# Kernel optimization log

Hardware: AMD Instinct MI355X
Metric: run time of the kernel (lower is better)

## Reference

```python
import jax, jax.numpy as jnp
import numpy as np

N_EMB = 384
BLOCK = 128

def setup_inputs() -> dict:
    key = jax.random.key(0)
    k1, k2, k3, k4 = jax.random.split(key, 4)
    B, T, hs = 1024, 128, 64
    x = jax.random.normal(k1, (B, T, N_EMB), dtype=jnp.float32)
    Wk = jax.random.normal(k2, (hs, N_EMB), dtype=jnp.float32) * (N_EMB ** -0.5)
    Wq = jax.random.normal(k3, (hs, N_EMB), dtype=jnp.float32) * (N_EMB ** -0.5)
    Wv = jax.random.normal(k4, (hs, N_EMB), dtype=jnp.float32) * (N_EMB ** -0.5)
    return {"x": x, "Wk": Wk, "Wq": Wq, "Wv": Wv}

def reference(x, Wk, Wq, Wv):
    B, T, C = x.shape
    # nn.Linear(n_emb, head_size, bias=False): y = x @ W.T
    k = jnp.einsum('btc,hc->bth', x, Wk)  # [B,T,hs]
    q = jnp.einsum('btc,hc->bth', x, Wq)
    v = jnp.einsum('btc,hc->bth', x, Wv)
    # NOTE: source scales by C**-0.5 where C = n_emb (384), not head_size
    w = jnp.einsum('bth,bsh->bts', q, k) * (C ** -0.5)  # [B,T,T]
    causal = jnp.tril(jnp.ones((T, T), dtype=bool))
    w = jnp.where(causal, w, -jnp.inf)
    w = jax.nn.softmax(w, axis=-1)
    # dropout is identity in eval mode
    out = jnp.einsum('bts,bsh->bth', w, v)  # [B,T,hs]
    return out
```

## Files before the change

kernel.cpp:

```cpp
#include <hip/hip_runtime.h>

typedef __bf16 bf16_t;
typedef __attribute__((ext_vector_type(8))) __bf16 bf16x8;
typedef __attribute__((ext_vector_type(4))) float floatx4;

#define MFMA16(a, b, c) __builtin_amdgcn_mfma_f32_16x16x32_bf16((a), (b), (c), 0, 0, 0)
#define GLOAD_LDS(g, l)                                                                      \
    __builtin_amdgcn_global_load_lds((const __attribute__((address_space(1))) unsigned int*)(g), \
                                     (__attribute__((address_space(3))) unsigned int*)(l), 16, 0, 0)

constexpr int TT = 128;
constexpr int CD = 384;
constexpr int HS = 64;
constexpr int BB = 1024;
constexpr int NCH = 12;

constexpr int XB0 = 0, XB1 = 17408, WB0 = 34816, WB1 = 47104;
constexpr int SMEM_BYTES = 59392;

constexpr int QK_STR = 72;
constexpr int VT_STR = 136;
constexpr int QS_OFF = 0;
constexpr int KS_OFF = TT * QK_STR;
constexpr int VT_OFF = 2 * TT * QK_STR;
constexpr int PS_OFF = 0;

__global__ void wconv_kernel(const float* __restrict__ wq, const float* __restrict__ wk,
                             const float* __restrict__ wv, bf16_t* __restrict__ wf) {
    const int t = blockIdx.x * 256 + threadIdx.x;
    if (t >= 144 * 64) return;
    const int lane = t & 63;
    const int f    = t >> 6;
    const int nt   = f & 3;
    const int proj = (f >> 2) % 3;
    const int kki  = f / 12;
    const float* W = (proj == 0) ? wq : ((proj == 1) ? wk : wv);
    const int h = 16 * nt + (lane & 15);
    const int c = 32 * kki + 8 * (lane >> 4);
    const float* src = W + h * CD + c;
    bf16x8 o;
#pragma unroll
    for (int j = 0; j < 8; ++j) o[j] = (bf16_t)src[j];
    *(bf16x8*)(wf + (size_t)t * 8) = o;
}

__launch_bounds__(256, 2)
__global__ void attn_kernel(const float* __restrict__ x, const bf16_t* __restrict__ wf,
                            float* __restrict__ out) {
    __shared__ __align__(16) char smem_raw[SMEM_BYTES];
    bf16_t* smem = (bf16_t*)smem_raw;
    const int b    = blockIdx.x;
    const int lane = threadIdx.x & 63;
    const int w    = threadIdx.x >> 6;
    const int l15  = lane & 15;
    const int g    = lane >> 4;
    const char* xb  = (const char*)(x + (size_t)b * TT * CD);
    const char* wfb = (const char*)wf;

    int      xi[5];
    unsigned xg[5];
#pragma unroll
    for (int t2 = 0; t2 < 5; ++t2) {
        const int i = w + 4 * t2;
        xi[t2] = i;
        unsigned u   = (unsigned)i * 1024u + (unsigned)lane * 16u;
        unsigned p   = u / 272u;
        unsigned rem = u - 272u * p;
        unsigned row = 2u * p + (rem >> 7);
        xg[t2] = (rem < 256u) ? row * (CD * 4u) + (rem & 127u) : 0u;
    }

    auto stage = [&](int c) {
        const char* xsrc = xb + c * 128;
        char*       xd   = smem_raw + ((c & 1) ? XB1 : XB0);
#pragma unroll
        for (int t2 = 0; t2 < 5; ++t2)
            if (xi[t2] <= 16) GLOAD_LDS(xsrc + xg[t2], xd + xi[t2] * 1024);
        const char* wsrc = wfb + (size_t)(c * 12 + 3 * w) * 1024 + (size_t)lane * 16;
        char*       wd   = smem_raw + ((c & 1) ? WB1 : WB0) + 3 * w * 1024;
#pragma unroll
        for (int j = 0; j < 3; ++j) GLOAD_LDS(wsrc + (size_t)j * 1024, wd + j * 1024);
    };

    floatx4 accq[2][4], acck[2][4], accv[2][4];
#pragma unroll
    for (int mt = 0; mt < 2; ++mt)
#pragma unroll
        for (int nt = 0; nt < 4; ++nt) {
            accq[mt][nt] = (floatx4)0.0f;
            acck[mt][nt] = (floatx4)0.0f;
            accv[mt][nt] = (floatx4)0.0f;
        }

    stage(0);
    __syncthreads();

    for (int c = 0; c < NCH; ++c) {
        if (c + 1 < NCH) stage(c + 1);

        const char*   xs = smem_raw + ((c & 1) ? XB1 : XB0);
        const char*   ws = smem_raw + ((c & 1) ? WB1 : WB0);

        bf16x8 a[2];
#pragma unroll
        for (int mt = 0; mt < 2; ++mt) {
            const int   R = 32 * w + 16 * mt + l15;
            const char* p = xs + (R >> 1) * 272 + (R & 1) * 128 + 32 * g;
            float4 f0 = *(const float4*)p;
            float4 f1 = *(const float4*)(p + 16);
            bf16x8 t;
            t[0] = (bf16_t)f0.x; t[1] = (bf16_t)f0.y; t[2] = (bf16_t)f0.z; t[3] = (bf16_t)f0.w;
            t[4] = (bf16_t)f1.x; t[5] = (bf16_t)f1.y; t[6] = (bf16_t)f1.z; t[7] = (bf16_t)f1.w;
            a[mt] = t;
        }
        bf16x8 wbf[12];
#pragma unroll
        for (int pn = 0; pn < 12; ++pn)
            wbf[pn] = *(const bf16x8*)(ws + pn * 1024 + lane * 16);
#pragma unroll
        for (int nt = 0; nt < 4; ++nt) {
            accq[0][nt] = MFMA16(a[0], wbf[0 + nt], accq[0][nt]);
            accq[1][nt] = MFMA16(a[1], wbf[0 + nt], accq[1][nt]);
            acck[0][nt] = MFMA16(a[0], wbf[4 + nt], acck[0][nt]);
            acck[1][nt] = MFMA16(a[1], wbf[4 + nt], acck[1][nt]);
            accv[0][nt] = MFMA16(a[0], wbf[8 + nt], accv[0][nt]);
            accv[1][nt] = MFMA16(a[1], wbf[8 + nt], accv[1][nt]);
        }
        __syncthreads();
    }

#pragma unroll
    for (int mt = 0; mt < 2; ++mt)
#pragma unroll
        for (int nt = 0; nt < 4; ++nt) {
            const int t0 = 32 * w + 16 * mt + 4 * g;
            const int h  = 16 * nt + l15;
#pragma unroll
            for (int r = 0; r < 4; ++r) {
                smem[QS_OFF + (t0 + r) * QK_STR + h] = (bf16_t)accq[mt][nt][r];
                smem[KS_OFF + (t0 + r) * QK_STR + h] = (bf16_t)acck[mt][nt][r];
                smem[VT_OFF + h * VT_STR + t0 + r]   = (bf16_t)accv[mt][nt][r];
            }
        }
    __syncthreads();

    floatx4 sacc[2][8];
#pragma unroll
    for (int mt = 0; mt < 2; ++mt)
#pragma unroll
        for (int nt = 0; nt < 8; ++nt) sacc[mt][nt] = (floatx4)0.0f;

#pragma unroll
    for (int kt = 0; kt < 2; ++kt) {
        const int hh = 32 * kt + 8 * g;
        bf16x8 aq[2];
        aq[0] = *(const bf16x8*)(smem + QS_OFF + (32 * w + l15) * QK_STR + hh);
        aq[1] = *(const bf16x8*)(smem + QS_OFF + (32 * w + 16 + l15) * QK_STR + hh);
#pragma unroll
        for (int nt = 0; nt < 8; ++nt) {
            if (16 * nt <= 32 * w + 31) {
                bf16x8 bk = *(const bf16x8*)(smem + KS_OFF + (16 * nt + l15) * QK_STR + hh);
                if (16 * nt <= 32 * w + 15) sacc[0][nt] = MFMA16(aq[0], bk, sacc[0][nt]);
                sacc[1][nt] = MFMA16(aq[1], bk, sacc[1][nt]);
            }
        }
    }
    __syncthreads();

    const float scale = 0.05103103630798287f;
#pragma unroll
    for (int mt = 0; mt < 2; ++mt) {
#pragma unroll
        for (int r = 0; r < 4; ++r) {
            const int t = 32 * w + 16 * mt + 4 * g + r;
            float vals[8];
            float vmax = -__builtin_inff();
#pragma unroll
            for (int nt = 0; nt < 8; ++nt) {
                const int s = 16 * nt + l15;
                float v = (s <= t) ? sacc[mt][nt][r] * scale : -__builtin_inff();
                vals[nt] = v;
                vmax = fmaxf(vmax, v);
            }
            vmax = fmaxf(vmax, __shfl_xor(vmax, 1));
            vmax = fmaxf(vmax, __shfl_xor(vmax, 2));
            vmax = fmaxf(vmax, __shfl_xor(vmax, 4));
            vmax = fmaxf(vmax, __shfl_xor(vmax, 8));
            float sum = 0.0f;
#pragma unroll
            for (int nt = 0; nt < 8; ++nt) {
                float e = __expf(vals[nt] - vmax);
                vals[nt] = e;
                sum += e;
            }
            sum += __shfl_xor(sum, 1);
            sum += __shfl_xor(sum, 2);
            sum += __shfl_xor(sum, 4);
            sum += __shfl_xor(sum, 8);
            const float inv = 1.0f / sum;
#pragma unroll
            for (int nt = 0; nt < 8; ++nt)
                smem[PS_OFF + t * VT_STR + 16 * nt + l15] = (bf16_t)(vals[nt] * inv);
        }
    }

    floatx4 oacc[2][4];
#pragma unroll
    for (int mt = 0; mt < 2; ++mt)
#pragma unroll
        for (int nt = 0; nt < 4; ++nt) oacc[mt][nt] = (floatx4)0.0f;

    for (int st = 0; st <= w; ++st) {
        const int ss = 32 * st + 8 * g;
        bf16x8 ap0 = *(const bf16x8*)(smem + PS_OFF + (32 * w + l15) * VT_STR + ss);
        bf16x8 ap1 = *(const bf16x8*)(smem + PS_OFF + (32 * w + 16 + l15) * VT_STR + ss);
#pragma unroll
        for (int nt = 0; nt < 4; ++nt) {
            bf16x8 bv = *(const bf16x8*)(smem + VT_OFF + (16 * nt + l15) * VT_STR + ss);
            oacc[0][nt] = MFMA16(ap0, bv, oacc[0][nt]);
            oacc[1][nt] = MFMA16(ap1, bv, oacc[1][nt]);
        }
    }

    float* ob = out + (size_t)b * TT * HS;
#pragma unroll
    for (int mt = 0; mt < 2; ++mt)
#pragma unroll
        for (int nt = 0; nt < 4; ++nt) {
            const int t0 = 32 * w + 16 * mt + 4 * g;
            const int h  = 16 * nt + l15;
#pragma unroll
            for (int r = 0; r < 4; ++r)
                ob[(size_t)(t0 + r) * HS + h] = oacc[mt][nt][r];
        }
}

extern "C" void kernel_launch(void* const* d_in, const int* in_sizes, int n_in,
                              void* d_out, int out_size, void* d_ws, size_t ws_size,
                              hipStream_t stream) {
    const float* x  = (const float*)d_in[0];
    const float* wk = (const float*)d_in[1];
    const float* wq = (const float*)d_in[2];
    const float* wv = (const float*)d_in[3];
    float* out = (float*)d_out;

    bf16_t* wf = (bf16_t*)d_ws;

    wconv_kernel<<<36, 256, 0, stream>>>(wq, wk, wv, wf);
    attn_kernel<<<BB, 256, 0, stream>>>(x, wf, out);
}
```

Baseline: 306.5 us.

## Make attention kernel persistent over two batches and prefetch the next batch's x

The grid is halved so each workgroup processes two batch elements in sequence. While the first batch is in its projection tail, the first x chunk of the second batch is prefetched into an extra LDS region, so the next projection can start without a cold load. The staging pipeline now uses explicit vmcnt waits and raw barriers, and prefetches two chunks ahead. LDS per block grows to about 75 KB, which may lower occupancy. The hand-tuned wait counts are fragile if the number of issued loads changes.

```diff
diff --git a/kernel.cpp b/kernel.cpp
--- a/kernel.cpp
+++ b/kernel.cpp
@@ -8,15 +8,20 @@
 #define GLOAD_LDS(g, l)                                                                      \
     __builtin_amdgcn_global_load_lds((const __attribute__((address_space(1))) unsigned int*)(g), \
                                      (__attribute__((address_space(3))) unsigned int*)(l), 16, 0, 0)
+#define WAITV(N) asm volatile("s_waitcnt vmcnt(" #N ")" ::: "memory")
+#define WAITL0() asm volatile("s_waitcnt lgkmcnt(0)" ::: "memory")
+#define BAR() __builtin_amdgcn_s_barrier()
+#define PIN() __builtin_amdgcn_sched_barrier(0)
 
 constexpr int TT = 128;
 constexpr int CD = 384;
 constexpr int HS = 64;
 constexpr int BB = 1024;
 constexpr int NCH = 12;
-
-constexpr int XB0 = 0, XB1 = 17408, WB0 = 34816, WB1 = 47104;
-constexpr int SMEM_BYTES = 59392;
+constexpr int GRID = 512;
+
+constexpr int XB0 = 0, XB1 = 17408, WB0 = 34816, WB1 = 47104, XPF = 59392;
+constexpr int SMEM_BYTES = 76800;
 
 constexpr int QK_STR = 72;
 constexpr int VT_STR = 136;
@@ -49,12 +54,10 @@
                             float* __restrict__ out) {
     __shared__ __align__(16) char smem_raw[SMEM_BYTES];
     bf16_t* smem = (bf16_t*)smem_raw;
-    const int b    = blockIdx.x;
     const int lane = threadIdx.x & 63;
     const int w    = threadIdx.x >> 6;
     const int l15  = lane & 15;
     const int g    = lane >> 4;
-    const char* xb  = (const char*)(x + (size_t)b * TT * CD);
     const char* wfb = (const char*)wf;
 
     int      xi[5];
@@ -70,169 +73,212 @@
         xg[t2] = (rem < 256u) ? row * (CD * 4u) + (rem & 127u) : 0u;
     }
 
-    auto stage = [&](int c) {
-        const char* xsrc = xb + c * 128;
-        char*       xd   = smem_raw + ((c & 1) ? XB1 : XB0);
+    auto stage_x = [&](const char* xsrc, int boff) {
+        char* xd = smem_raw + boff;
 #pragma unroll
         for (int t2 = 0; t2 < 5; ++t2)
             if (xi[t2] <= 16) GLOAD_LDS(xsrc + xg[t2], xd + xi[t2] * 1024);
+    };
+    auto stage_w = [&](int c, int boff) {
         const char* wsrc = wfb + (size_t)(c * 12 + 3 * w) * 1024 + (size_t)lane * 16;
-        char*       wd   = smem_raw + ((c & 1) ? WB1 : WB0) + 3 * w * 1024;
+        char*       wd   = smem_raw + boff + 3 * w * 1024;
 #pragma unroll
         for (int j = 0; j < 3; ++j) GLOAD_LDS(wsrc + (size_t)j * 1024, wd + j * 1024);
     };
 
-    floatx4 accq[2][4], acck[2][4], accv[2][4];
-#pragma unroll
-    for (int mt = 0; mt < 2; ++mt)
-#pragma unroll
-        for (int nt = 0; nt < 4; ++nt) {
-            accq[mt][nt] = (floatx4)0.0f;
-            acck[mt][nt] = (floatx4)0.0f;
-            accv[mt][nt] = (floatx4)0.0f;
-        }
-
-    stage(0);
-    __syncthreads();
-
-    for (int c = 0; c < NCH; ++c) {
-        if (c + 1 < NCH) stage(c + 1);
-
-        const char*   xs = smem_raw + ((c & 1) ? XB1 : XB0);
-        const char*   ws = smem_raw + ((c & 1) ? WB1 : WB0);
-
-        bf16x8 a[2];
+    const char* xb0 = (const char*)(x + (size_t)blockIdx.x * TT * CD);
+    const char* xb1 = (const char*)(x + (size_t)(blockIdx.x + GRID) * TT * CD);
+
+    stage_x(xb0, XB0);
+    stage_w(0, WB0);
+    PIN();
+    stage_x(xb0 + 128, XB1);
+    stage_w(1, WB1);
+
+#pragma unroll 1
+    for (int it = 0; it < 2; ++it) {
+        const int   b    = blockIdx.x + it * GRID;
+        const char* xcur = it ? xb1 : xb0;
+
+        floatx4 accq[2][4], acck[2][4], accv[2][4];
+#pragma unroll
+        for (int mt = 0; mt < 2; ++mt)
+#pragma unroll
+            for (int nt = 0; nt < 4; ++nt) {
+                accq[mt][nt] = (floatx4)0.0f;
+                acck[mt][nt] = (floatx4)0.0f;
+                accv[mt][nt] = (floatx4)0.0f;
+            }
+
+        if (w == 0) WAITV(8); else WAITV(7);
+        BAR();
+
+#pragma unroll 1
+        for (int c = 0; c < NCH; ++c) {
+            const char* xs = (it == 1 && c == 0) ? smem_raw + XPF
+                                                 : smem_raw + ((c & 1) ? XB1 : XB0);
+            const char* ws = smem_raw + ((c & 1) ? WB1 : WB0);
+
+            bf16x8 a[2];
+#pragma unroll
+            for (int mt = 0; mt < 2; ++mt) {
+                const int   R = 32 * w + 16 * mt + l15;
+                const char* p = xs + (R >> 1) * 272 + (R & 1) * 128 + 32 * g;
+                float4 f0 = *(const float4*)p;
+                float4 f1 = *(const float4*)(p + 16);
+                bf16x8 t;
+                t[0] = (bf16_t)f0.x; t[1] = (bf16_t)f0.y; t[2] = (bf16_t)f0.z; t[3] = (bf16_t)f0.w;
+                t[4] = (bf16_t)f1.x; t[5] = (bf16_t)f1.y; t[6] = (bf16_t)f1.z; t[7] = (bf16_t)f1.w;
+                a[mt] = t;
+            }
+            bf16x8 wbf[12];
+#pragma unroll
+            for (int pn = 0; pn < 12; ++pn)
+                wbf[pn] = *(const bf16x8*)(ws + pn * 1024 + lane * 16);
+#pragma unroll
+            for (int nt = 0; nt < 4; ++nt) {
+                accq[0][nt] = MFMA16(a[0], wbf[0 + nt], accq[0][nt]);
+                accq[1][nt] = MFMA16(a[1], wbf[0 + nt], accq[1][nt]);
+                acck[0][nt] = MFMA16(a[0], wbf[4 + nt], acck[0][nt]);
+                acck[1][nt] = MFMA16(a[1], wbf[4 + nt], acck[1][nt]);
+                accv[0][nt] = MFMA16(a[0], wbf[8 + nt], accv[0][nt]);
+                accv[1][nt] = MFMA16(a[1], wbf[8 + nt], accv[1][nt]);
+            }
+
+            WAITL0();
+            BAR();
+            if (c <= 9) {
+                stage_x(xcur + (c + 2) * 128, (c & 1) ? XB1 : XB0);
+                stage_w(c + 2, (c & 1) ? WB1 : WB0);
+                if (w == 0) WAITV(8); else WAITV(7);
+                BAR();
+            } else if (c == 10) {
+                if (it == 0) {
+                    stage_x(xb1, XPF);
+                    if (w == 0) WAITV(5); else WAITV(4);
+                } else {
+                    WAITV(0);
+                }
+                BAR();
+            }
+        }
+
+#pragma unroll
+        for (int mt = 0; mt < 2; ++mt)
+#pragma unroll
+            for (int nt = 0; nt < 4; ++nt) {
+                const int t0 = 32 * w + 16 * mt + 4 * g;
+                const int h  = 16 * nt + l15;
+#pragma unroll
+                for (int r = 0; r < 4; ++r) {
+                    smem[QS_OFF + (t0 + r) * QK_STR + h] = (bf16_t)accq[mt][nt][r];
+                    smem[KS_OFF + (t0 + r) * QK_STR + h] = (bf16_t)acck[mt][nt][r];
+                    smem[VT_OFF + h * VT_STR + t0 + r]   = (bf16_t)accv[mt][nt][r];
+                }
+            }
+        WAITL0();
+        BAR();
+
+        floatx4 sacc[2][8];
+#pragma unroll
+        for (int mt = 0; mt < 2; ++mt)
+#pragma unroll
+            for (int nt = 0; nt < 8; ++nt) sacc[mt][nt] = (floatx4)0.0f;
+
+#pragma unroll
+        for (int kt = 0; kt < 2; ++kt) {
+            const int hh = 32 * kt + 8 * g;
+            bf16x8 aq[2];
+            aq[0] = *(const bf16x8*)(smem + QS_OFF + (32 * w + l15) * QK_STR + hh);
+            aq[1] = *(const bf16x8*)(smem + QS_OFF + (32 * w + 16 + l15) * QK_STR + hh);
+#pragma unroll
+            for (int nt = 0; nt < 8; ++nt) {
+                if (16 * nt <= 32 * w + 31) {
+                    bf16x8 bk = *(const bf16x8*)(smem + KS_OFF + (16 * nt + l15) * QK_STR + hh);
+                    if (16 * nt <= 32 * w + 15) sacc[0][nt] = MFMA16(aq[0], bk, sacc[0][nt]);
+                    sacc[1][nt] = MFMA16(aq[1], bk, sacc[1][nt]);
+                }
+            }
+        }
+        WAITL0();
+        BAR();
+
+        const float scale = 0.05103103630798287f;
 #pragma unroll
         for (int mt = 0; mt < 2; ++mt) {
-            const int   R = 32 * w + 16 * mt + l15;
-            const char* p = xs + (R >> 1) * 272 + (R & 1) * 128 + 32 * g;
-            float4 f0 = *(const float4*)p;
-            float4 f1 = *(const float4*)(p + 16);
-            bf16x8 t;
-            t[0] = (bf16_t)f0.x; t[1] = (bf16_t)f0.y; t[2] = (bf16_t)f0.z; t[3] = (bf16_t)f0.w;
-            t[4] = (bf16_t)f1.x; t[5] = (bf16_t)f1.y; t[6] = (bf16_t)f1.z; t[7] = (bf16_t)f1.w;
-            a[mt] = t;
-        }
-        bf16x8 wbf[12];
-#pragma unroll
-        for (int pn = 0; pn < 12; ++pn)
-            wbf[pn] = *(const bf16x8*)(ws + pn * 1024 + lane * 16);
-#pragma unroll
-        for (int nt = 0; nt < 4; ++nt) {
-            accq[0][nt] = MFMA16(a[0], wbf[0 + nt], accq[0][nt]);
-            accq[1][nt] = MFMA16(a[1], wbf[0 + nt], accq[1][nt]);
-            acck[0][nt] = MFMA16(a[0], wbf[4 + nt], acck[0][nt]);
-            acck[1][nt] = MFMA16(a[1], wbf[4 + nt], acck[1][nt]);
-            accv[0][nt] = MFMA16(a[0], wbf[8 + nt], accv[0][nt]);
-            accv[1][nt] = MFMA16(a[1], wbf[8 + nt], accv[1][nt]);
-        }
-        __syncthreads();
+#pragma unroll
+            for (int r = 0; r < 4; ++r) {
+                const int t = 32 * w + 16 * mt + 4 * g + r;
+                float vals[8];
+                float vmax = -__builtin_inff();
+#pragma unroll
+                for (int nt = 0; nt < 8; ++nt) {
+                    const int s = 16 * nt + l15;
+                    float v = (s <= t) ? sacc[mt][nt][r] * scale : -__builtin_inff();
+                    vals[nt] = v;
+                    vmax = fmaxf(vmax, v);
+                }
+                vmax = fmaxf(vmax, __shfl_xor(vmax, 1));
+                vmax = fmaxf(vmax, __shfl_xor(vmax, 2));
+                vmax = fmaxf(vmax, __shfl_xor(vmax, 4));
+                vmax = fmaxf(vmax, __shfl_xor(vmax, 8));
+                float sum = 0.0f;
+#pragma unroll
+                for (int nt = 0; nt < 8; ++nt) {
+                    float e = __expf(vals[nt] - vmax);
+                    vals[nt] = e;
+                    sum += e;
+                }
+                sum += __shfl_xor(sum, 1);
+                sum += __shfl_xor(sum, 2);
+                sum += __shfl_xor(sum, 4);
+                sum += __shfl_xor(sum, 8);
+                const float inv = 1.0f / sum;
+#pragma unroll
+                for (int nt = 0; nt < 8; ++nt)
+                    smem[PS_OFF + t * VT_STR + 16 * nt + l15] = (bf16_t)(vals[nt] * inv);
+            }
+        }
+
+        floatx4 oacc[2][4];
+#pragma unroll
+        for (int mt = 0; mt < 2; ++mt)
+#pragma unroll
+            for (int nt = 0; nt < 4; ++nt) oacc[mt][nt] = (floatx4)0.0f;
+
+        for (int st = 0; st <= w; ++st) {
+            const int ss = 32 * st + 8 * g;
+            bf16x8 ap0 = *(const bf16x8*)(smem + PS_OFF + (32 * w + l15) * VT_STR + ss);
+            bf16x8 ap1 = *(const bf16x8*)(smem + PS_OFF + (32 * w + 16 + l15) * VT_STR + ss);
+#pragma unroll
+            for (int nt = 0; nt < 4; ++nt) {
+                bf16x8 bv = *(const bf16x8*)(smem + VT_OFF + (16 * nt + l15) * VT_STR + ss);
+                oacc[0][nt] = MFMA16(ap0, bv, oacc[0][nt]);
+                oacc[1][nt] = MFMA16(ap1, bv, oacc[1][nt]);
+            }
+        }
+
+        float* ob = out + (size_t)b * TT * HS;
+#pragma unroll
+        for (int mt = 0; mt < 2; ++mt)
+#pragma unroll
+            for (int nt = 0; nt < 4; ++nt) {
+                const int t0 = 32 * w + 16 * mt + 4 * g;
+                const int h  = 16 * nt + l15;
+#pragma unroll
+                for (int r = 0; r < 4; ++r)
+                    ob[(size_t)(t0 + r) * HS + h] = oacc[mt][nt][r];
+            }
+
+        if (it == 0) {
+            WAITL0();
+            BAR();
+            stage_w(0, WB0);
+            PIN();
+            stage_x(xb1 + 128, XB1);
+            stage_w(1, WB1);
+        }
     }
-
-#pragma unroll
-    for (int mt = 0; mt < 2; ++mt)
-#pragma unroll
-        for (int nt = 0; nt < 4; ++nt) {
-            const int t0 = 32 * w + 16 * mt + 4 * g;
-            const int h  = 16 * nt + l15;
-#pragma unroll
-            for (int r = 0; r < 4; ++r) {
-                smem[QS_OFF + (t0 + r) * QK_STR + h] = (bf16_t)accq[mt][nt][r];
-                smem[KS_OFF + (t0 + r) * QK_STR + h] = (bf16_t)acck[mt][nt][r];
-                smem[VT_OFF + h * VT_STR + t0 + r]   = (bf16_t)accv[mt][nt][r];
-            }
-        }
-    __syncthreads();
-
-    floatx4 sacc[2][8];
-#pragma unroll
-    for (int mt = 0; mt < 2; ++mt)
-#pragma unroll
-        for (int nt = 0; nt < 8; ++nt) sacc[mt][nt] = (floatx4)0.0f;
-
-#pragma unroll
-    for (int kt = 0; kt < 2; ++kt) {
-        const int hh = 32 * kt + 8 * g;
-        bf16x8 aq[2];
-        aq[0] = *(const bf16x8*)(smem + QS_OFF + (32 * w + l15) * QK_STR + hh);
-        aq[1] = *(const bf16x8*)(smem + QS_OFF + (32 * w + 16 + l15) * QK_STR + hh);
-#pragma unroll
-        for (int nt = 0; nt < 8; ++nt) {
-            if (16 * nt <= 32 * w + 31) {
-                bf16x8 bk = *(const bf16x8*)(smem + KS_OFF + (16 * nt + l15) * QK_STR + hh);
-                if (16 * nt <= 32 * w + 15) sacc[0][nt] = MFMA16(aq[0], bk, sacc[0][nt]);
-                sacc[1][nt] = MFMA16(aq[1], bk, sacc[1][nt]);
-            }
-        }
-    }
-    __syncthreads();
-
-    const float scale = 0.05103103630798287f;
-#pragma unroll
-    for (int mt = 0; mt < 2; ++mt) {
-#pragma unroll
-        for (int r = 0; r < 4; ++r) {
-            const int t = 32 * w + 16 * mt + 4 * g + r;
-            float vals[8];
-            float vmax = -__builtin_inff();
-#pragma unroll
-            for (int nt = 0; nt < 8; ++nt) {
-                const int s = 16 * nt + l15;
-                float v = (s <= t) ? sacc[mt][nt][r] * scale : -__builtin_inff();
-                vals[nt] = v;
-                vmax = fmaxf(vmax, v);
-            }
-            vmax = fmaxf(vmax, __shfl_xor(vmax, 1));
-            vmax = fmaxf(vmax, __shfl_xor(vmax, 2));
-            vmax = fmaxf(vmax, __shfl_xor(vmax, 4));
-            vmax = fmaxf(vmax, __shfl_xor(vmax, 8));
-            float sum = 0.0f;
-#pragma unroll
-            for (int nt = 0; nt < 8; ++nt) {
-                float e = __expf(vals[nt] - vmax);
-                vals[nt] = e;
-                sum += e;
-            }
-            sum += __shfl_xor(sum, 1);
-            sum += __shfl_xor(sum, 2);
-            sum += __shfl_xor(sum, 4);
-            sum += __shfl_xor(sum, 8);
-            const float inv = 1.0f / sum;
-#pragma unroll
-            for (int nt = 0; nt < 8; ++nt)
-                smem[PS_OFF + t * VT_STR + 16 * nt + l15] = (bf16_t)(vals[nt] * inv);
-        }
-    }
-
-    floatx4 oacc[2][4];
-#pragma unroll
-    for (int mt = 0; mt < 2; ++mt)
-#pragma unroll
-        for (int nt = 0; nt < 4; ++nt) oacc[mt][nt] = (floatx4)0.0f;
-
-    for (int st = 0; st <= w; ++st) {
-        const int ss = 32 * st + 8 * g;
-        bf16x8 ap0 = *(const bf16x8*)(smem + PS_OFF + (32 * w + l15) * VT_STR + ss);
-        bf16x8 ap1 = *(const bf16x8*)(smem + PS_OFF + (32 * w + 16 + l15) * VT_STR + ss);
-#pragma unroll
-        for (int nt = 0; nt < 4; ++nt) {
-            bf16x8 bv = *(const bf16x8*)(smem + VT_OFF + (16 * nt + l15) * VT_STR + ss);
-            oacc[0][nt] = MFMA16(ap0, bv, oacc[0][nt]);
-            oacc[1][nt] = MFMA16(ap1, bv, oacc[1][nt]);
-        }
-    }
-
-    float* ob = out + (size_t)b * TT * HS;
-#pragma unroll
-    for (int mt = 0; mt < 2; ++mt)
-#pragma unroll
-        for (int nt = 0; nt < 4; ++nt) {
-            const int t0 = 32 * w + 16 * mt + 4 * g;
-            const int h  = 16 * nt + l15;
-#pragma unroll
-            for (int r = 0; r < 4; ++r)
-                ob[(size_t)(t0 + r) * HS + h] = oacc[mt][nt][r];
-        }
 }
 
 extern "C" void kernel_launch(void* const* d_in, const int* in_sizes, int n_in,
@@ -247,5 +293,5 @@
     bf16_t* wf = (bf16_t*)d_ws;
 
     wconv_kernel<<<36, 256, 0, stream>>>(wq, wk, wv, wf);
-    attn_kernel<<<BB, 256, 0, stream>>>(x, wf, out);
+    attn_kernel<<<GRID, 256, 0, stream>>>(x, wf, out);
 }
```

New measurement: 304.2 us. Within noise of the previous version (-0.7%).

## Make attention kernel persistent with register-resident weights and pipelined x staging

Applied to the files above, without the earlier changes.

Switches to a persistent grid of 256 blocks of 512 threads, each processing four batches. Projection weights are loaded into registers once per block. x is streamed in 32-row chunks through swizzled double-buffered LDS with explicit vmcnt waits. This removes repeated weight staging and overlaps the next batch's loads with attention compute. In exchange it uses very large LDS and many registers (likely one block per CU), and the Q/K/V region aliases the second x buffer.

```diff
diff --git a/kernel.cpp b/kernel.cpp
--- a/kernel.cpp
+++ b/kernel.cpp
@@ -8,22 +8,26 @@
 #define GLOAD_LDS(g, l)                                                                      \
     __builtin_amdgcn_global_load_lds((const __attribute__((address_space(1))) unsigned int*)(g), \
                                      (__attribute__((address_space(3))) unsigned int*)(l), 16, 0, 0)
+#define WAITV(N) asm volatile("s_waitcnt vmcnt(" #N ")" ::: "memory")
+#define WAITL0() asm volatile("s_waitcnt lgkmcnt(0)" ::: "memory")
+#define BAR() __builtin_amdgcn_s_barrier()
+#define PIN() __builtin_amdgcn_sched_barrier(0)
 
 constexpr int TT = 128;
 constexpr int CD = 384;
 constexpr int HS = 64;
-constexpr int BB = 1024;
-constexpr int NCH = 12;
-
-constexpr int XB0 = 0, XB1 = 17408, WB0 = 34816, WB1 = 47104;
-constexpr int SMEM_BYTES = 59392;
-
+constexpr int GRID = 256;
+constexpr int XCHUNK = 32 * CD * 4;
+
+constexpr int XB0 = 0, XB1 = XCHUNK;
+constexpr int OVB = 2 * XCHUNK;
 constexpr int QK_STR = 72;
 constexpr int VT_STR = 136;
-constexpr int QS_OFF = 0;
-constexpr int KS_OFF = TT * QK_STR;
-constexpr int VT_OFF = 2 * TT * QK_STR;
-constexpr int PS_OFF = 0;
+constexpr int QS_OFF = OVB / 2;
+constexpr int KS_OFF = QS_OFF + TT * QK_STR;
+constexpr int VT_OFF = QS_OFF + 2 * TT * QK_STR;
+constexpr int PS_OFF = QS_OFF;
+constexpr int SMEM_BYTES = OVB + 2 * (2 * TT * QK_STR + 64 * VT_STR);
 
 __global__ void wconv_kernel(const float* __restrict__ wq, const float* __restrict__ wk,
                              const float* __restrict__ wv, bf16_t* __restrict__ wf) {
@@ -44,141 +48,128 @@
     *(bf16x8*)(wf + (size_t)t * 8) = o;
 }
 
-__launch_bounds__(256, 2)
+__launch_bounds__(512, 2)
 __global__ void attn_kernel(const float* __restrict__ x, const bf16_t* __restrict__ wf,
                             float* __restrict__ out) {
     __shared__ __align__(16) char smem_raw[SMEM_BYTES];
     bf16_t* smem = (bf16_t*)smem_raw;
-    const int b    = blockIdx.x;
     const int lane = threadIdx.x & 63;
     const int w    = threadIdx.x >> 6;
     const int l15  = lane & 15;
     const int g    = lane >> 4;
-    const char* xb  = (const char*)(x + (size_t)b * TT * CD);
+    const int cg   = w >> 1;
+    const int mh   = w & 1;
     const char* wfb = (const char*)wf;
 
-    int      xi[5];
-    unsigned xg[5];
-#pragma unroll
-    for (int t2 = 0; t2 < 5; ++t2) {
-        const int i = w + 4 * t2;
-        xi[t2] = i;
-        unsigned u   = (unsigned)i * 1024u + (unsigned)lane * 16u;
-        unsigned p   = u / 272u;
-        unsigned rem = u - 272u * p;
-        unsigned row = 2u * p + (rem >> 7);
-        xg[t2] = (rem < 256u) ? row * (CD * 4u) + (rem & 127u) : 0u;
+    bf16x8 wreg[36];
+#pragma unroll
+    for (int kk = 0; kk < 12; ++kk)
+#pragma unroll
+        for (int pj = 0; pj < 3; ++pj)
+            wreg[kk * 3 + pj] =
+                *(const bf16x8*)(wfb + ((size_t)((kk * 3 + pj) * 4 + cg) << 10) + lane * 16);
+
+    unsigned soff[6];
+#pragma unroll
+    for (int t = 0; t < 6; ++t) {
+        unsigned L  = (unsigned)(w * 6 + t) * 1024u + (unsigned)lane * 16u;
+        unsigned r  = L / 1536u;
+        unsigned gL = (L - r * 1536u) >> 4;
+        soff[t] = r * 1536u + ((gL ^ (r & 7u)) << 4);
     }
-
-    auto stage = [&](int c) {
-        const char* xsrc = xb + c * 128;
-        char*       xd   = smem_raw + ((c & 1) ? XB1 : XB0);
-#pragma unroll
-        for (int t2 = 0; t2 < 5; ++t2)
-            if (xi[t2] <= 16) GLOAD_LDS(xsrc + xg[t2], xd + xi[t2] * 1024);
-        const char* wsrc = wfb + (size_t)(c * 12 + 3 * w) * 1024 + (size_t)lane * 16;
-        char*       wd   = smem_raw + ((c & 1) ? WB1 : WB0) + 3 * w * 1024;
-#pragma unroll
-        for (int j = 0; j < 3; ++j) GLOAD_LDS(wsrc + (size_t)j * 1024, wd + j * 1024);
+    auto stage = [&](const char* gsrc, char* lds) {
+#pragma unroll
+        for (int t = 0; t < 6; ++t) GLOAD_LDS(gsrc + soff[t], lds + (w * 6 + t) * 1024);
     };
 
-    floatx4 accq[2][4], acck[2][4], accv[2][4];
-#pragma unroll
-    for (int mt = 0; mt < 2; ++mt)
-#pragma unroll
-        for (int nt = 0; nt < 4; ++nt) {
-            accq[mt][nt] = (floatx4)0.0f;
-            acck[mt][nt] = (floatx4)0.0f;
-            accv[mt][nt] = (floatx4)0.0f;
-        }
-
-    stage(0);
-    __syncthreads();
-
-    for (int c = 0; c < NCH; ++c) {
-        if (c + 1 < NCH) stage(c + 1);
-
-        const char*   xs = smem_raw + ((c & 1) ? XB1 : XB0);
-        const char*   ws = smem_raw + ((c & 1) ? WB1 : WB0);
-
-        bf16x8 a[2];
-#pragma unroll
-        for (int mt = 0; mt < 2; ++mt) {
-            const int   R = 32 * w + 16 * mt + l15;
-            const char* p = xs + (R >> 1) * 272 + (R & 1) * 128 + 32 * g;
-            float4 f0 = *(const float4*)p;
-            float4 f1 = *(const float4*)(p + 16);
-            bf16x8 t;
-            t[0] = (bf16_t)f0.x; t[1] = (bf16_t)f0.y; t[2] = (bf16_t)f0.z; t[3] = (bf16_t)f0.w;
-            t[4] = (bf16_t)f1.x; t[5] = (bf16_t)f1.y; t[6] = (bf16_t)f1.z; t[7] = (bf16_t)f1.w;
-            a[mt] = t;
-        }
-        bf16x8 wbf[12];
-#pragma unroll
-        for (int pn = 0; pn < 12; ++pn)
-            wbf[pn] = *(const bf16x8*)(ws + pn * 1024 + lane * 16);
-#pragma unroll
-        for (int nt = 0; nt < 4; ++nt) {
-            accq[0][nt] = MFMA16(a[0], wbf[0 + nt], accq[0][nt]);
-            accq[1][nt] = MFMA16(a[1], wbf[0 + nt], accq[1][nt]);
-            acck[0][nt] = MFMA16(a[0], wbf[4 + nt], acck[0][nt]);
-            acck[1][nt] = MFMA16(a[1], wbf[4 + nt], acck[1][nt]);
-            accv[0][nt] = MFMA16(a[0], wbf[8 + nt], accv[0][nt]);
-            accv[1][nt] = MFMA16(a[1], wbf[8 + nt], accv[1][nt]);
-        }
-        __syncthreads();
-    }
-
-#pragma unroll
-    for (int mt = 0; mt < 2; ++mt)
-#pragma unroll
-        for (int nt = 0; nt < 4; ++nt) {
-            const int t0 = 32 * w + 16 * mt + 4 * g;
-            const int h  = 16 * nt + l15;
-#pragma unroll
-            for (int r = 0; r < 4; ++r) {
-                smem[QS_OFF + (t0 + r) * QK_STR + h] = (bf16_t)accq[mt][nt][r];
-                smem[KS_OFF + (t0 + r) * QK_STR + h] = (bf16_t)acck[mt][nt][r];
-                smem[VT_OFF + h * VT_STR + t0 + r]   = (bf16_t)accv[mt][nt][r];
-            }
-        }
-    __syncthreads();
-
-    floatx4 sacc[2][8];
-#pragma unroll
-    for (int mt = 0; mt < 2; ++mt)
-#pragma unroll
-        for (int nt = 0; nt < 8; ++nt) sacc[mt][nt] = (floatx4)0.0f;
-
-#pragma unroll
-    for (int kt = 0; kt < 2; ++kt) {
-        const int hh = 32 * kt + 8 * g;
-        bf16x8 aq[2];
-        aq[0] = *(const bf16x8*)(smem + QS_OFF + (32 * w + l15) * QK_STR + hh);
-        aq[1] = *(const bf16x8*)(smem + QS_OFF + (32 * w + 16 + l15) * QK_STR + hh);
-#pragma unroll
-        for (int nt = 0; nt < 8; ++nt) {
-            if (16 * nt <= 32 * w + 31) {
-                bf16x8 bk = *(const bf16x8*)(smem + KS_OFF + (16 * nt + l15) * QK_STR + hh);
-                if (16 * nt <= 32 * w + 15) sacc[0][nt] = MFMA16(aq[0], bk, sacc[0][nt]);
-                sacc[1][nt] = MFMA16(aq[1], bk, sacc[1][nt]);
-            }
-        }
-    }
-    __syncthreads();
-
-    const float scale = 0.05103103630798287f;
-#pragma unroll
-    for (int mt = 0; mt < 2; ++mt) {
+    const int      R   = 16 * mh + l15;
+    const unsigned xro = (unsigned)R * 1536u + (unsigned)(((2 * g) ^ (R & 7)) << 4);
+
+    auto compute_chunk = [&](int c, const char* xs) {
+        floatx4 acc0 = (floatx4)0.0f, acc1 = (floatx4)0.0f, acc2 = (floatx4)0.0f;
+#pragma unroll
+        for (int kk = 0; kk < 12; ++kk) {
+            const unsigned a0 = xro + 128u * kk;
+            float4 f0 = *(const float4*)(xs + a0);
+            float4 f1 = *(const float4*)(xs + (a0 ^ 16u));
+            bf16x8 a;
+            a[0] = (bf16_t)f0.x; a[1] = (bf16_t)f0.y; a[2] = (bf16_t)f0.z; a[3] = (bf16_t)f0.w;
+            a[4] = (bf16_t)f1.x; a[5] = (bf16_t)f1.y; a[6] = (bf16_t)f1.z; a[7] = (bf16_t)f1.w;
+            acc0 = MFMA16(a, wreg[kk * 3 + 0], acc0);
+            acc1 = MFMA16(a, wreg[kk * 3 + 1], acc1);
+            acc2 = MFMA16(a, wreg[kk * 3 + 2], acc2);
+        }
+        const int t0 = 32 * c + 16 * mh + 4 * g;
+        const int h  = 16 * cg + l15;
+#pragma unroll
+        for (int ri = 0; ri < 4; ++ri) {
+            smem[QS_OFF + (t0 + ri) * QK_STR + h] = (bf16_t)acc0[ri];
+            smem[KS_OFF + (t0 + ri) * QK_STR + h] = (bf16_t)acc1[ri];
+            smem[VT_OFF + h * VT_STR + (t0 + ri)] = (bf16_t)acc2[ri];
+        }
+    };
+
+    const char* xbase = (const char*)x;
+    const char* xb00  = xbase + (size_t)blockIdx.x * TT * CD * 4;
+
+    stage(xb00, smem_raw + XB0);
+    PIN();
+    stage(xb00 + XCHUNK, smem_raw + XB1);
+
+#pragma unroll 1
+    for (int it = 0; it < 4; ++it) {
+        const int   b  = blockIdx.x + GRID * it;
+        const char* xb = xbase + (size_t)b * TT * CD * 4;
+        const char* xn = xb + (size_t)GRID * TT * CD * 4;
+
+        WAITV(6); BAR();
+        compute_chunk(0, smem_raw + XB0);
+        WAITL0(); BAR();
+        stage(xb + 2 * XCHUNK, smem_raw + XB0);
+        WAITV(6); BAR();
+        compute_chunk(1, smem_raw + XB1);
+        WAITL0(); BAR();
+        stage(xb + 3 * XCHUNK, smem_raw + XB1);
+        WAITV(6); BAR();
+        compute_chunk(2, smem_raw + XB0);
+        WAITL0(); BAR();
+        if (it < 3) {
+            stage(xn, smem_raw + XB0);
+            WAITV(6);
+        } else {
+            WAITV(0);
+        }
+        BAR();
+        compute_chunk(3, smem_raw + XB1);
+        WAITL0(); BAR();
+
+        floatx4 sacc[8];
+#pragma unroll
+        for (int nt = 0; nt < 8; ++nt) sacc[nt] = (floatx4)0.0f;
+#pragma unroll
+        for (int kt = 0; kt < 2; ++kt) {
+            const int hh = 32 * kt + 8 * g;
+            bf16x8 aq = *(const bf16x8*)(smem + QS_OFF + (16 * w + l15) * QK_STR + hh);
+#pragma unroll
+            for (int nt = 0; nt < 8; ++nt) {
+                if (nt <= w) {
+                    bf16x8 bk = *(const bf16x8*)(smem + KS_OFF + (16 * nt + l15) * QK_STR + hh);
+                    sacc[nt] = MFMA16(aq, bk, sacc[nt]);
+                }
+            }
+        }
+        WAITL0(); BAR();
+
+        const float scale = 0.05103103630798287f;
 #pragma unroll
         for (int r = 0; r < 4; ++r) {
-            const int t = 32 * w + 16 * mt + 4 * g + r;
+            const int t = 16 * w + 4 * g + r;
             float vals[8];
             float vmax = -__builtin_inff();
 #pragma unroll
             for (int nt = 0; nt < 8; ++nt) {
                 const int s = 16 * nt + l15;
-                float v = (s <= t) ? sacc[mt][nt][r] * scale : -__builtin_inff();
+                float v = (s <= t) ? sacc[nt][r] * scale : -__builtin_inff();
                 vals[nt] = v;
                 vmax = fmaxf(vmax, v);
             }
@@ -202,37 +193,35 @@
             for (int nt = 0; nt < 8; ++nt)
                 smem[PS_OFF + t * VT_STR + 16 * nt + l15] = (bf16_t)(vals[nt] * inv);
         }
+
+        floatx4 oacc[4];
+#pragma unroll
+        for (int nt = 0; nt < 4; ++nt) oacc[nt] = (floatx4)0.0f;
+#pragma unroll
+        for (int st = 0; st < 4; ++st) {
+            if (st <= (w >> 1)) {
+                const int ss = 32 * st + 8 * g;
+                bf16x8 ap = *(const bf16x8*)(smem + PS_OFF + (16 * w + l15) * VT_STR + ss);
+#pragma unroll
+                for (int nt = 0; nt < 4; ++nt) {
+                    bf16x8 bv = *(const bf16x8*)(smem + VT_OFF + (16 * nt + l15) * VT_STR + ss);
+                    oacc[nt] = MFMA16(ap, bv, oacc[nt]);
+                }
+            }
+        }
+
+        float* ob = out + (size_t)b * TT * HS;
+#pragma unroll
+        for (int nt = 0; nt < 4; ++nt)
+#pragma unroll
+            for (int r = 0; r < 4; ++r)
+                ob[(size_t)(16 * w + 4 * g + r) * HS + 16 * nt + l15] = oacc[nt][r];
+
+        if (it < 3) {
+            PIN();
+            stage(xn + XCHUNK, smem_raw + XB1);
+        }
     }
-
-    floatx4 oacc[2][4];
-#pragma unroll
-    for (int mt = 0; mt < 2; ++mt)
-#pragma unroll
-        for (int nt = 0; nt < 4; ++nt) oacc[mt][nt] = (floatx4)0.0f;
-
-    for (int st = 0; st <= w; ++st) {
-        const int ss = 32 * st + 8 * g;
-        bf16x8 ap0 = *(const bf16x8*)(smem + PS_OFF + (32 * w + l15) * VT_STR + ss);
-        bf16x8 ap1 = *(const bf16x8*)(smem + PS_OFF + (32 * w + 16 + l15) * VT_STR + ss);
-#pragma unroll
-        for (int nt = 0; nt < 4; ++nt) {
-            bf16x8 bv = *(const bf16x8*)(smem + VT_OFF + (16 * nt + l15) * VT_STR + ss);
-            oacc[0][nt] = MFMA16(ap0, bv, oacc[0][nt]);
-            oacc[1][nt] = MFMA16(ap1, bv, oacc[1][nt]);
-        }
-    }
-
-    float* ob = out + (size_t)b * TT * HS;
-#pragma unroll
-    for (int mt = 0; mt < 2; ++mt)
-#pragma unroll
-        for (int nt = 0; nt < 4; ++nt) {
-            const int t0 = 32 * w + 16 * mt + 4 * g;
-            const int h  = 16 * nt + l15;
-#pragma unroll
-            for (int r = 0; r < 4; ++r)
-                ob[(size_t)(t0 + r) * HS + h] = oacc[mt][nt][r];
-        }
 }
 
 extern "C" void kernel_launch(void* const* d_in, const int* in_sizes, int n_in,
@@ -247,5 +236,5 @@
     bf16_t* wf = (bf16_t*)d_ws;
 
     wconv_kernel<<<36, 256, 0, stream>>>(wq, wk, wv, wf);
-    attn_kernel<<<BB, 256, 0, stream>>>(x, wf, out);
+    attn_kernel<<<GRID, 512, 0, stream>>>(x, wf, out);
 }
```

Result: slower. 430.6 us (+40.5%).

## Read projection weights from global, prefetch x two chunks ahead, raise occupancy

Applied to the files above, without the earlier changes.

The projection weights are no longer staged through LDS; each wave reads its bf16 weight fragments straight from global memory, where they are shared by all blocks and should stay cached. That frees LDS, so the x double buffer becomes a depth-two prefetch managed with manual waitcnt and barriers instead of __syncthreads, and launch bounds rise to three blocks per CU. The intent is to cut LDS traffic and barrier cost and to hide latency through more resident blocks. The risk is that waiting on the weight loads' vmcnt also forces the x prefetch to finish early, which weakens the overlap, and per-lane global weight loads add L2 traffic.

```diff
diff --git a/kernel.cpp b/kernel.cpp
--- a/kernel.cpp
+++ b/kernel.cpp
@@ -8,6 +8,10 @@
 #define GLOAD_LDS(g, l)                                                                      \
     __builtin_amdgcn_global_load_lds((const __attribute__((address_space(1))) unsigned int*)(g), \
                                      (__attribute__((address_space(3))) unsigned int*)(l), 16, 0, 0)
+#define WAITV(N) asm volatile("s_waitcnt vmcnt(" #N ")" ::: "memory")
+#define WAITL0() asm volatile("s_waitcnt lgkmcnt(0)" ::: "memory")
+#define BAR() __builtin_amdgcn_s_barrier()
+#define PIN() __builtin_amdgcn_sched_barrier(0)
 
 constexpr int TT = 128;
 constexpr int CD = 384;
@@ -15,15 +19,14 @@
 constexpr int BB = 1024;
 constexpr int NCH = 12;
 
-constexpr int XB0 = 0, XB1 = 17408, WB0 = 34816, WB1 = 47104;
-constexpr int SMEM_BYTES = 59392;
-
+constexpr int XB0 = 0, XB1 = 17408;
 constexpr int QK_STR = 72;
 constexpr int VT_STR = 136;
 constexpr int QS_OFF = 0;
 constexpr int KS_OFF = TT * QK_STR;
 constexpr int VT_OFF = 2 * TT * QK_STR;
 constexpr int PS_OFF = 0;
+constexpr int SMEM_BYTES = 2 * (VT_OFF + 64 * VT_STR);
 
 __global__ void wconv_kernel(const float* __restrict__ wq, const float* __restrict__ wk,
                              const float* __restrict__ wv, bf16_t* __restrict__ wf) {
@@ -44,17 +47,15 @@
     *(bf16x8*)(wf + (size_t)t * 8) = o;
 }
 
-__launch_bounds__(256, 2)
+__launch_bounds__(256, 3)
 __global__ void attn_kernel(const float* __restrict__ x, const bf16_t* __restrict__ wf,
                             float* __restrict__ out) {
     __shared__ __align__(16) char smem_raw[SMEM_BYTES];
     bf16_t* smem = (bf16_t*)smem_raw;
-    const int b    = blockIdx.x;
     const int lane = threadIdx.x & 63;
     const int w    = threadIdx.x >> 6;
     const int l15  = lane & 15;
     const int g    = lane >> 4;
-    const char* xb  = (const char*)(x + (size_t)b * TT * CD);
     const char* wfb = (const char*)wf;
 
     int      xi[5];
@@ -70,17 +71,18 @@
         xg[t2] = (rem < 256u) ? row * (CD * 4u) + (rem & 127u) : 0u;
     }
 
-    auto stage = [&](int c) {
-        const char* xsrc = xb + c * 128;
-        char*       xd   = smem_raw + ((c & 1) ? XB1 : XB0);
+    auto stage_x = [&](const char* xsrc, int boff) {
+        char* xd = smem_raw + boff;
 #pragma unroll
         for (int t2 = 0; t2 < 5; ++t2)
             if (xi[t2] <= 16) GLOAD_LDS(xsrc + xg[t2], xd + xi[t2] * 1024);
-        const char* wsrc = wfb + (size_t)(c * 12 + 3 * w) * 1024 + (size_t)lane * 16;
-        char*       wd   = smem_raw + ((c & 1) ? WB1 : WB0) + 3 * w * 1024;
-#pragma unroll
-        for (int j = 0; j < 3; ++j) GLOAD_LDS(wsrc + (size_t)j * 1024, wd + j * 1024);
     };
+
+    const char* xb = (const char*)(x + (size_t)blockIdx.x * TT * CD);
+
+    stage_x(xb, XB0);
+    PIN();
+    stage_x(xb + 128, XB1);
 
     floatx4 accq[2][4], acck[2][4], accv[2][4];
 #pragma unroll
@@ -92,14 +94,12 @@
             accv[mt][nt] = (floatx4)0.0f;
         }
 
-    stage(0);
-    __syncthreads();
-
+    if (w == 0) WAITV(5); else WAITV(4);
+    BAR();
+
+#pragma unroll 1
     for (int c = 0; c < NCH; ++c) {
-        if (c + 1 < NCH) stage(c + 1);
-
-        const char*   xs = smem_raw + ((c & 1) ? XB1 : XB0);
-        const char*   ws = smem_raw + ((c & 1) ? WB1 : WB0);
+        const char* xs = smem_raw + ((c & 1) ? XB1 : XB0);
 
         bf16x8 a[2];
 #pragma unroll
@@ -113,10 +113,11 @@
             t[4] = (bf16_t)f1.x; t[5] = (bf16_t)f1.y; t[6] = (bf16_t)f1.z; t[7] = (bf16_t)f1.w;
             a[mt] = t;
         }
+        const char* wsrc = wfb + (size_t)(c * 12) * 1024 + (size_t)lane * 16;
         bf16x8 wbf[12];
 #pragma unroll
         for (int pn = 0; pn < 12; ++pn)
-            wbf[pn] = *(const bf16x8*)(ws + pn * 1024 + lane * 16);
+            wbf[pn] = *(const bf16x8*)(wsrc + pn * 1024);
 #pragma unroll
         for (int nt = 0; nt < 4; ++nt) {
             accq[0][nt] = MFMA16(a[0], wbf[0 + nt], accq[0][nt]);
@@ -126,7 +127,13 @@
             accv[0][nt] = MFMA16(a[0], wbf[8 + nt], accv[0][nt]);
             accv[1][nt] = MFMA16(a[1], wbf[8 + nt], accv[1][nt]);
         }
-        __syncthreads();
+
+        WAITL0();
+        BAR();
+        if (c <= 9) {
+            PIN();
+            stage_x(xb + (c + 2) * 128, (c & 1) ? XB1 : XB0);
+        }
     }
 
 #pragma unroll
@@ -142,7 +149,8 @@
                 smem[VT_OFF + h * VT_STR + t0 + r]   = (bf16_t)accv[mt][nt][r];
             }
         }
-    __syncthreads();
+    WAITL0();
+    BAR();
 
     floatx4 sacc[2][8];
 #pragma unroll
@@ -165,7 +173,7 @@
             }
         }
     }
-    __syncthreads();
+    WAITL0(); BAR();
 
     const float scale = 0.05103103630798287f;
 #pragma unroll
@@ -222,7 +230,7 @@
         }
     }
 
-    float* ob = out + (size_t)b * TT * HS;
+    float* ob = out + (size_t)blockIdx.x * TT * HS;
 #pragma unroll
     for (int mt = 0; mt < 2; ++mt)
 #pragma unroll
```

Measured after the change: 318.0 us. 3.8% more time.
